# Optimization experiments

Measured on AMD Instinct MI355X. Metric: run time of the kernel, lower is better.

The kernel has to match this reference:

```python
import jax, jax.numpy as jnp
import numpy as np

D = 1024
H = 16
HD = D // H
S = 2048
B = 4
EPS = 1e-5


def gelu_tanh(x):
    c = jnp.sqrt(2.0 / jnp.pi).astype(x.dtype)
    return 0.5 * x * (1.0 + jnp.tanh(c * (x + 0.044715 * x ** 3)))


def layernorm(x, gamma, beta):
    mu = jnp.mean(x, axis=-1, keepdims=True)
    var = jnp.var(x, axis=-1, keepdims=True)
    return (x - mu) * jax.lax.rsqrt(var + EPS) * gamma + beta


def setup_inputs() -> dict:
    key = jax.random.key(0)
    ks = jax.random.split(key, 12)
    s = 0.02
    return {
        "x": jax.random.normal(ks[0], (B, S, D), jnp.float32),
        "Wq": jax.random.normal(ks[1], (D, D), jnp.float32) * s,
        "Wk": jax.random.normal(ks[2], (D, D), jnp.float32) * s,
        "Wv": jax.random.normal(ks[3], (D, D), jnp.float32) * s,
        "Wo": jax.random.normal(ks[4], (D, D), jnp.float32) * s,
        "bo": jnp.zeros((D,), jnp.float32),
        "W1": jax.random.normal(ks[5], (D, 4 * D), jnp.float32) * s,
        "b1": jnp.zeros((4 * D,), jnp.float32),
        "W2": jax.random.normal(ks[6], (4 * D, D), jnp.float32) * s,
        "b2": jnp.zeros((D,), jnp.float32),
        "g1": jnp.ones((D,), jnp.float32),
        "be1": jnp.zeros((D,), jnp.float32),
        "g2": jnp.ones((D,), jnp.float32),
        "be2": jnp.zeros((D,), jnp.float32),
    }


def reference(x, Wq, Wk, Wv, Wo, bo, W1, b1, W2, b2, g1, be1, g2, be2):
    b, n, d = x.shape
    # --- attention sub-block (pre-LN) ---
    h = layernorm(x, g1, be1)
    q = (h @ Wq).reshape(b, n, H, HD).transpose(0, 2, 1, 3)  # [b,H,n,hd]
    k = (h @ Wk).reshape(b, n, H, HD).transpose(0, 2, 1, 3)
    v = (h @ Wv).reshape(b, n, H, HD).transpose(0, 2, 1, 3)
    scores = jnp.einsum('bhqd,bhkd->bhqk', q, k) / jnp.sqrt(jnp.float32(HD))
    causal = jnp.tril(jnp.ones((n, n), dtype=bool))
    scores = jnp.where(causal, scores, -jnp.inf)
    w = jax.nn.softmax(scores, axis=-1)  # dropout rate 0 -> identity
    attn = jnp.einsum('bhqk,bhkd->bhqd', w, v)
    attn = attn.transpose(0, 2, 1, 3).reshape(b, n, d)
    x = x + (attn @ Wo + bo)
    # --- FFN sub-block (pre-LN) ---
    h = layernorm(x, g2, be2)
    h = gelu_tanh(h @ W1 + b1) @ W2 + b2
    return x + h
```

## Files before the change

kernel.cpp:

```cpp
#include <hip/hip_runtime.h>
#include <hip/hip_bf16.h>
#include <math.h>


typedef __attribute__((ext_vector_type(8))) short bf16x8;
typedef __attribute__((ext_vector_type(4))) float f32x4;

#define AS1 __attribute__((address_space(1)))
#define AS3 __attribute__((address_space(3)))

__device__ __forceinline__ void gl_lds16(const void* g, void* l) {
  __builtin_amdgcn_global_load_lds((const AS1 void*)g, (AS3 void*)l, 16, 0, 0);
}

__device__ __forceinline__ float gelu_f(float x) {
  const float c = 0.7978845608028654f;
  return 0.5f * x * (1.0f + tanhf(c * (x + 0.044715f * x * x * x)));
}

__device__ __forceinline__ float bf2f(short s) {
  unsigned u = ((unsigned)(unsigned short)s) << 16;
  return __builtin_bit_cast(float, u);
}
__device__ __forceinline__ short f2bf(float f) {
  __hip_bfloat16 h = __float2bfloat16(f);
  return __builtin_bit_cast(short, h);
}

__global__ void __launch_bounds__(256) tcvt_all(
    const float* __restrict__ Wq, const float* __restrict__ Wk,
    const float* __restrict__ Wv, const float* __restrict__ Wo,
    const float* __restrict__ W1, const float* __restrict__ W2,
    __hip_bfloat16* __restrict__ WqkvT, __hip_bfloat16* __restrict__ WoT,
    __hip_bfloat16* __restrict__ W1T, __hip_bfloat16* __restrict__ W2T) {
  __shared__ float t[32][33];
  const int bid = blockIdx.x;
  const float* W;
  __hip_bfloat16* WT;
  int K, N, n0, k0;
  if (bid < 4096) {
    const int which = bid >> 10, r = bid & 1023;
    K = 1024; N = 1024;
    n0 = (r & 31) * 32; k0 = (r >> 5) * 32;
    W = which == 0 ? Wq : which == 1 ? Wk : which == 2 ? Wv : Wo;
    WT = which < 3 ? WqkvT + which * 1024 * 1024 : WoT;
  } else if (bid < 8192) {
    const int r = bid - 4096;
    K = 1024; N = 4096;
    n0 = (r & 127) * 32; k0 = (r >> 7) * 32;
    W = W1; WT = W1T;
  } else {
    const int r = bid - 8192;
    K = 4096; N = 1024;
    n0 = (r & 31) * 32; k0 = (r >> 5) * 32;
    W = W2; WT = W2T;
  }
  const int tx = threadIdx.x, ty0 = threadIdx.y;
#pragma unroll
  for (int i = 0; i < 4; i++) {
    int ty = ty0 + i * 8;
    t[ty][tx] = W[(size_t)(k0 + ty) * N + n0 + tx];
  }
  __syncthreads();
#pragma unroll
  for (int i = 0; i < 4; i++) {
    int ty = ty0 + i * 8;
    WT[(size_t)(n0 + ty) * K + k0 + tx] = __float2bfloat16(t[tx][ty]);
  }
}

__global__ void __launch_bounds__(256) vtr_kernel(
    const __hip_bfloat16* __restrict__ qkv, __hip_bfloat16* __restrict__ vt) {
  __shared__ __hip_bfloat16 t[32][33];
  const int s0 = blockIdx.x * 32;
  const int hd0 = blockIdx.y * 32;
  const int bh = blockIdx.z;
  const int b = bh >> 4, h = bh & 15;
  const int tx = threadIdx.x, ty0 = threadIdx.y;
  const __hip_bfloat16* src =
      qkv + (size_t)(b * 2048 + s0) * 3072 + 2048 + h * 64 + hd0;
#pragma unroll
  for (int i = 0; i < 4; i++) {
    int ty = ty0 + i * 8;
    t[ty][tx] = src[(size_t)ty * 3072 + tx];
  }
  __syncthreads();
  __hip_bfloat16* dst = vt + ((size_t)bh * 64 + hd0) * 2048 + s0;
#pragma unroll
  for (int i = 0; i < 4; i++) {
    int ty = ty0 + i * 8;
    dst[(size_t)ty * 2048 + tx] = t[tx][ty];
  }
}

__global__ void __launch_bounds__(256) ln_kernel(
    const float* __restrict__ x, const float* __restrict__ gma,
    const float* __restrict__ bta, __hip_bfloat16* __restrict__ out) {
  const int row = blockIdx.x;
  const int tid = threadIdx.x;
  const float4 v = ((const float4*)(x + (size_t)row * 1024))[tid];
  float s = v.x + v.y + v.z + v.w;
  float s2 = v.x * v.x + v.y * v.y + v.z * v.z + v.w * v.w;
#pragma unroll
  for (int m = 32; m; m >>= 1) {
    s += __shfl_xor(s, m);
    s2 += __shfl_xor(s2, m);
  }
  __shared__ float red[8];
  const int w = tid >> 6, lane = tid & 63;
  if (lane == 0) { red[w] = s; red[4 + w] = s2; }
  __syncthreads();
  s = red[0] + red[1] + red[2] + red[3];
  s2 = red[4] + red[5] + red[6] + red[7];
  const float mu = s * (1.0f / 1024.0f);
  const float var = s2 * (1.0f / 1024.0f) - mu * mu;
  const float rs = rsqrtf(var + 1e-5f);
  const float4 gv = ((const float4*)gma)[tid];
  const float4 bv = ((const float4*)bta)[tid];
  __hip_bfloat16* orow = out + (size_t)row * 1024 + tid * 4;
  orow[0] = __float2bfloat16((v.x - mu) * rs * gv.x + bv.x);
  orow[1] = __float2bfloat16((v.y - mu) * rs * gv.y + bv.y);
  orow[2] = __float2bfloat16((v.z - mu) * rs * gv.z + bv.z);
  orow[3] = __float2bfloat16((v.w - mu) * rs * gv.w + bv.w);
}

template <int BM, int BN, int EPI>
__global__ void __launch_bounds__(512, 2) gemm8(
    const __hip_bfloat16* __restrict__ Ap, const __hip_bfloat16* __restrict__ Bp,
    void* __restrict__ outp, const float* __restrict__ bias,
    const float* __restrict__ resid, int N, int K) {
  constexpr int PM = BM / 2;
  constexpr int MR = PM / 16;
  constexpr int NPH = MR / 2;
  constexpr int HA = BM / 128;
  constexpr int ABYTES = BM * 128;
  constexpr int BUFB = ABYTES + BN * 128;
  __shared__ __attribute__((aligned(128))) char smem[2 * BUFB];

  const int tid = threadIdx.x;
  const int lane = tid & 63, w = tid >> 6;
  const int wr = w >> 2, wc = w & 3;
  const int cr = lane & 15, g = lane >> 4;

  const int gx = gridDim.x;
  const int nwg = gx * gridDim.y;
  const int orig = blockIdx.y * gx + blockIdx.x;
  const int f = (orig & 7) * (nwg >> 3) + (orig >> 3);
  const int sid = f >> 4, wit = f & 15;
  const int stm = gx >> 2;
  const int bm = (sid % stm) * 4 + (wit & 3);
  const int bn = (sid / stm) * 4 + (wit >> 2);
  const int bmr = bm * BM, bnr = bn * BN;
  const int nkt = K >> 6;

  const int srow8 = lane >> 3;
  const int ssl = ((lane & 7) ^ srow8) * 8;
  unsigned aofs[2][2], bofs[2][2];
#pragma unroll
  for (int h = 0; h < 2; h++)
#pragma unroll
    for (int c = 0; c < 2; c++) {
      const int ha = (h < HA) ? h : 0;
      aofs[h][c] =
          (unsigned)(((bmr + ha * 128 + (w + c * 8) * 8 + srow8) * K + ssl) * 2);
      bofs[h][c] =
          (unsigned)(((bnr + h * 128 + (w + c * 8) * 8 + srow8) * K + ssl) * 2);
    }

  const int rk = cr & 7;
  const char* aP[2][2];
  const char* bP[2][2];
#pragma unroll
  for (int bf = 0; bf < 2; bf++)
#pragma unroll
    for (int ks = 0; ks < 2; ks++) {
      aP[bf][ks] =
          smem + bf * BUFB + (wr * PM + cr) * 128 + ((ks * 4 + g) ^ rk) * 16;
      bP[bf][ks] = smem + bf * BUFB + ABYTES + (wc * 64 + cr) * 128 +
                   ((ks * 4 + g) ^ rk) * 16;
    }

#define STG_A(BUF, tt, h)                                                     \
  do {                                                                        \
    const unsigned col = (unsigned)(tt) * 128u;                               \
    gl_lds16((const char*)Ap + aofs[h][0] + col,                              \
             smem + (BUF) * BUFB + (h) * 16384 + w * 1024);                   \
    gl_lds16((const char*)Ap + aofs[h][1] + col,                              \
             smem + (BUF) * BUFB + (h) * 16384 + (w + 8) * 1024);             \
  } while (0)
#define STG_B(BUF, tt, h)                                                     \
  do {                                                                        \
    const unsigned col = (unsigned)(tt) * 128u;                               \
    gl_lds16((const char*)Bp + bofs[h][0] + col,                              \
             smem + (BUF) * BUFB + ABYTES + (h) * 16384 + w * 1024);          \
    gl_lds16((const char*)Bp + bofs[h][1] + col,                              \
             smem + (BUF) * BUFB + ABYTES + (h) * 16384 + (w + 8) * 1024);    \
  } while (0)

  f32x4 acc[MR][4];
#pragma unroll
  for (int i = 0; i < MR; i++)
#pragma unroll
    for (int j = 0; j < 4; j++) acc[i][j] = (f32x4){0.f, 0.f, 0.f, 0.f};
  bf16x8 bv[4][2];

#pragma unroll
  for (int h = 0; h < HA; h++) STG_A(0, 0, h);
  STG_B(0, 0, 0); STG_B(0, 0, 1);
  STG_B(1, 1, 0); STG_B(1, 1, 1);

#define TILE_BODY(BUF, t)                                                     \
  {                                                                           \
    asm volatile("s_waitcnt vmcnt(4)" ::: "memory");                          \
    __builtin_amdgcn_s_barrier();                                             \
    const int tA = ((t) + 1 < nkt) ? (t) + 1 : (t) - 1;                       \
    const int tB = ((t) + 2 < nkt) ? (t) + 2 : (t);                           \
    _Pragma("unroll") for (int q = 0; q < NPH; q++) {                         \
      bf16x8 av[2][2];                                                        \
      _Pragma("unroll") for (int mm = 0; mm < 2; mm++)                        \
          _Pragma("unroll") for (int ks = 0; ks < 2; ks++) av[mm][ks] =       \
          *(const bf16x8*)(aP[BUF][ks] + (q * 2 + mm) * 2048);                \
      if (q == 0) {                                                           \
        _Pragma("unroll") for (int n = 0; n < 4; n++)                         \
            _Pragma("unroll") for (int ks = 0; ks < 2; ks++) bv[n][ks] =      \
            *(const bf16x8*)(bP[BUF][ks] + n * 2048);                         \
      }                                                                       \
      if constexpr (NPH == 4) {                                               \
        if (q == 0) { STG_A((BUF) ^ 1, tA, 0); }                              \
        else if (q == 1) { STG_A((BUF) ^ 1, tA, 1); }                         \
        else if (q == 2) { STG_B(BUF, tB, 0); }                               \
        else { STG_B(BUF, tB, 1); }                                           \
      } else {                                                                \
        if (q == 0) { STG_A((BUF) ^ 1, tA, 0); }                              \
        else { STG_B(BUF, tB, 0); STG_B(BUF, tB, 1); }                        \
      }                                                                       \
      __builtin_amdgcn_s_barrier();                                           \
      asm volatile("s_waitcnt lgkmcnt(0)" ::: "memory");                      \
      __builtin_amdgcn_s_setprio(1);                                          \
      _Pragma("unroll") for (int mm = 0; mm < 2; mm++)                        \
          _Pragma("unroll") for (int n = 0; n < 4; n++)                       \
              _Pragma("unroll") for (int ks = 0; ks < 2; ks++)                \
                  acc[q * 2 + mm][n] =                                        \
          __builtin_amdgcn_mfma_f32_16x16x32_bf16(av[mm][ks], bv[n][ks],      \
                                                  acc[q * 2 + mm][n], 0, 0, 0); \
      __builtin_amdgcn_s_setprio(0);                                          \
    }                                                                         \
  }

  for (int t = 0; t < nkt; t += 2) {
    TILE_BODY(0, t)
    TILE_BODY(1, t + 1)
  }
  asm volatile("s_waitcnt vmcnt(0)" ::: "memory");

#pragma unroll
  for (int m = 0; m < MR; m++) {
#pragma unroll
    for (int rr = 0; rr < 4; rr++) {
      const int row = bmr + wr * PM + m * 16 + g * 4 + rr;
#pragma unroll
      for (int n = 0; n < 4; n++) {
        const int col = bnr + wc * 64 + n * 16 + cr;
        float v = acc[m][n][rr];
        if (EPI == 0) {
          ((__hip_bfloat16*)outp)[(size_t)row * N + col] = __float2bfloat16(v);
        } else if (EPI == 1) {
          v += bias[col] + resid[(size_t)row * N + col];
          ((float*)outp)[(size_t)row * N + col] = v;
        } else {
          v = gelu_f(v + bias[col]);
          ((__hip_bfloat16*)outp)[(size_t)row * N + col] = __float2bfloat16(v);
        }
      }
    }
  }
#undef STG_A
#undef STG_B
#undef TILE_BODY
}

template <int EPI>
__global__ void __launch_bounds__(256) gemm97(
    const __hip_bfloat16* __restrict__ Ap, const __hip_bfloat16* __restrict__ Bp,
    void* __restrict__ outp, const float* __restrict__ bias,
    const float* __restrict__ resid, int N, int K) {
  __shared__ __hip_bfloat16 sA[128 * 64];
  __shared__ __hip_bfloat16 sB[128 * 64];
  const int tid = threadIdx.x;
  const int lane = tid & 63, w = tid >> 6;
  const int wr = w >> 1, wc = w & 1;
  const int cr = lane & 15, g = lane >> 4;

  const int gx = gridDim.x;
  const int nwg = gx * gridDim.y;
  const int orig = blockIdx.y * gx + blockIdx.x;
  const int f = (orig & 7) * (nwg >> 3) + (orig >> 3);
  const int sid = f >> 4, wit = f & 15;
  const int stm = gx >> 2;
  const int bm = (sid % stm) * 4 + (wit & 3);
  const int bn = (sid / stm) * 4 + (wit >> 2);
  const int bmr = bm * 128, bnr = bn * 128;

  const int l8 = lane >> 3;
  const int ssl = ((lane & 7) ^ l8) * 8;
  const int rk = cr & 7;

  f32x4 acc[4][4];
#pragma unroll
  for (int i = 0; i < 4; i++)
#pragma unroll
    for (int j = 0; j < 4; j++) acc[i][j] = (f32x4){0.f, 0.f, 0.f, 0.f};

  for (int k0 = 0; k0 < K; k0 += 64) {
#pragma unroll
    for (int i = 0; i < 4; i++) {
      const int chunk = w * 4 + i;
      const int row = chunk * 8 + l8;
      gl_lds16(Ap + (size_t)(bmr + row) * K + k0 + ssl, sA + chunk * 512);
      gl_lds16(Bp + (size_t)(bnr + row) * K + k0 + ssl, sB + chunk * 512);
    }
    __syncthreads();
#pragma unroll
    for (int ks = 0; ks < 2; ks++) {
      bf16x8 a[4], b[4];
#pragma unroll
      for (int m = 0; m < 4; m++)
        a[m] = *(const bf16x8*)(sA + (wr * 64 + m * 16 + cr) * 64 +
                                ((ks * 4 + g) ^ rk) * 8);
#pragma unroll
      for (int n = 0; n < 4; n++)
        b[n] = *(const bf16x8*)(sB + (wc * 64 + n * 16 + cr) * 64 +
                                ((ks * 4 + g) ^ rk) * 8);
#pragma unroll
      for (int m = 0; m < 4; m++)
#pragma unroll
        for (int n = 0; n < 4; n++)
          acc[m][n] =
              __builtin_amdgcn_mfma_f32_16x16x32_bf16(a[m], b[n], acc[m][n], 0, 0, 0);
    }
    __syncthreads();
  }

#pragma unroll
  for (int m = 0; m < 4; m++) {
#pragma unroll
    for (int rr = 0; rr < 4; rr++) {
      const int row = bmr + wr * 64 + m * 16 + g * 4 + rr;
#pragma unroll
      for (int n = 0; n < 4; n++) {
        const int col = bnr + wc * 64 + n * 16 + cr;
        float v = acc[m][n][rr];
        if (EPI == 0) {
          ((__hip_bfloat16*)outp)[(size_t)row * N + col] = __float2bfloat16(v);
        } else if (EPI == 1) {
          v += bias[col] + resid[(size_t)row * N + col];
          ((float*)outp)[(size_t)row * N + col] = v;
        } else {
          v = gelu_f(v + bias[col]);
          ((__hip_bfloat16*)outp)[(size_t)row * N + col] = __float2bfloat16(v);
        }
      }
    }
  }
}

__global__ void __launch_bounds__(256) attn_kernel(
    const __hip_bfloat16* __restrict__ qkv, const __hip_bfloat16* __restrict__ vt,
    __hip_bfloat16* __restrict__ o) {
  __shared__ __hip_bfloat16 sK[2][64 * 64];
  __shared__ __hip_bfloat16 sV[2][64 * 64];
  __shared__ __hip_bfloat16 pl[4][16][64];
  const int tid = threadIdx.x, lane = tid & 63, w = tid >> 6;
  const int bid = blockIdx.x;
  const int bh = (bid & 7) + 8 * ((bid >> 3) & 7);
  const int qt = 15 - (bid >> 6);
  const int b = bh >> 4, h = bh & 15;
  const int cr = lane & 15, g = lane >> 4;
  const int qr0 = qt * 128 + w * 32;
  const float NEG = -1e30f;
  const float SC2 = 0.18033688011112042f;
  const int sw = cr & 7;
  const int sg0 = (g ^ sw) * 8;
  const int sg1 = ((g ^ sw) ^ 4) * 8;
  const int pkey = (cr & 7) << 1;

  bf16x8 aq[2][2];
#pragma unroll
  for (int m = 0; m < 2; m++) {
    const __hip_bfloat16* qp =
        qkv + (size_t)(b * 2048 + qr0 + m * 16 + cr) * 3072 + h * 64 + g * 8;
    bf16x8 q0 = *(const bf16x8*)qp;
    bf16x8 q1 = *(const bf16x8*)(qp + 32);
#pragma unroll
    for (int j = 0; j < 8; j++) {
      aq[m][0][j] = f2bf(bf2f(q0[j]) * SC2);
      aq[m][1][j] = f2bf(bf2f(q1[j]) * SC2);
    }
  }
  const __hip_bfloat16* kbase = qkv + (size_t)(b * 2048) * 3072 + 1024 + h * 64;
  const __hip_bfloat16* vbase = vt + (size_t)bh * 64 * 2048;

  const int l8 = lane >> 3, c8 = lane & 7;
  const int c8s = (c8 ^ l8) * 8;
#define STAGE_TILE(bi, ktile)                                                   \
  {                                                                             \
    _Pragma("unroll") for (int i = 0; i < 2; i++) {                             \
      const int rb = (i * 4 + w) * 8 + l8;                                      \
      gl_lds16(kbase + (size_t)((ktile) * 64 + rb) * 3072 + c8s,                \
               &sK[bi][(i * 4 + w) * 512]);                                     \
      gl_lds16(vbase + (size_t)rb * 2048 + (ktile) * 64 + c8s,                  \
               &sV[bi][(i * 4 + w) * 512]);                                     \
    }                                                                           \
  }

  f32x4 oacc[2][4];
#pragma unroll
  for (int m = 0; m < 2; m++)
#pragma unroll
    for (int i = 0; i < 4; i++) oacc[m][i] = (f32x4){0.f, 0.f, 0.f, 0.f};
  float mrow[2] = {NEG, NEG};
  float lrow[2] = {0.f, 0.f};

  const int nkt = (qt + 1) * 2;
  STAGE_TILE(0, 0);
  asm volatile("s_waitcnt vmcnt(0)" ::: "memory");
  __syncthreads();
  int cur = 0;

  for (int kt = 0; kt < nkt; ++kt) {
    if (kt + 1 < nkt) STAGE_TILE(cur ^ 1, kt + 1);

    if (kt * 64 <= qr0 + 31) {
      f32x4 st[4][2];
      __builtin_amdgcn_s_setprio(1);
#pragma unroll
      for (int kf = 0; kf < 4; kf++) {
        const bf16x8 bk0 = *(const bf16x8*)&sK[cur][(kf * 16 + cr) * 64 + sg0];
        const bf16x8 bk1 = *(const bf16x8*)&sK[cur][(kf * 16 + cr) * 64 + sg1];
#pragma unroll
        for (int mq = 0; mq < 2; mq++) {
          f32x4 z = (f32x4){0.f, 0.f, 0.f, 0.f};
          z = __builtin_amdgcn_mfma_f32_16x16x32_bf16(bk0, aq[mq][0], z, 0, 0, 0);
          z = __builtin_amdgcn_mfma_f32_16x16x32_bf16(bk1, aq[mq][1], z, 0, 0, 0);
          st[kf][mq] = z;
        }
      }
      __builtin_amdgcn_s_setprio(0);
      if (kt * 64 + 63 > qr0) {
#pragma unroll
        for (int kf = 0; kf < 4; kf++)
#pragma unroll
          for (int mq = 0; mq < 2; mq++)
#pragma unroll
            for (int rr = 0; rr < 4; rr++) {
              const int kvcol = kt * 64 + kf * 16 + g * 4 + rr;
              const int qrow = qr0 + mq * 16 + cr;
              if (kvcol > qrow) st[kf][mq][rr] = NEG;
            }
      }
#pragma unroll
      for (int mq = 0; mq < 2; mq++) {
        float pmax = st[0][mq][0];
#pragma unroll
        for (int kf = 0; kf < 4; kf++)
#pragma unroll
          for (int rr = 0; rr < 4; rr++)
            pmax = fmaxf(pmax, st[kf][mq][rr]);
        pmax = fmaxf(pmax, __shfl_xor(pmax, 16));
        pmax = fmaxf(pmax, __shfl_xor(pmax, 32));
        if (__any(pmax > mrow[mq] + 8.0f)) {
          const float mn = fmaxf(mrow[mq], pmax);
          const float scl = exp2f(mrow[mq] - mn);
          mrow[mq] = mn;
          lrow[mq] *= scl;
          float s0 = __shfl(scl, g * 4 + 0);
          float s1 = __shfl(scl, g * 4 + 1);
          float s2 = __shfl(scl, g * 4 + 2);
          float s3 = __shfl(scl, g * 4 + 3);
#pragma unroll
          for (int nf = 0; nf < 4; nf++) {
            f32x4 t = oacc[mq][nf];
            t[0] *= s0; t[1] *= s1; t[2] *= s2; t[3] *= s3;
            oacc[mq][nf] = t;
          }
        }
        float rsum = 0.f;
#pragma unroll
        for (int kf = 0; kf < 4; kf++) {
          short4 pk;
#pragma unroll
          for (int rr = 0; rr < 4; rr++) {
            const float p = exp2f(st[kf][mq][rr] - mrow[mq]);
            rsum += p;
            ((short*)&pk)[rr] = f2bf(p);
          }
          const int slot4 = (kf * 4 + g) ^ pkey;
          *(short4*)&pl[w][cr][slot4 * 4] = pk;
        }
        rsum += __shfl_xor(rsum, 16);
        rsum += __shfl_xor(rsum, 32);
        lrow[mq] += rsum;
        const bf16x8 pa0 = *(const bf16x8*)&pl[w][cr][((2 * g) ^ pkey) * 4];
        const bf16x8 pa1 = *(const bf16x8*)&pl[w][cr][((2 * g + 8) ^ pkey) * 4];
        __builtin_amdgcn_s_setprio(1);
#pragma unroll
        for (int nf = 0; nf < 4; nf++) {
          const bf16x8 bv0 = *(const bf16x8*)&sV[cur][(nf * 16 + cr) * 64 + sg0];
          const bf16x8 bv1 = *(const bf16x8*)&sV[cur][(nf * 16 + cr) * 64 + sg1];
          oacc[mq][nf] = __builtin_amdgcn_mfma_f32_16x16x32_bf16(pa0, bv0, oacc[mq][nf], 0, 0, 0);
          oacc[mq][nf] = __builtin_amdgcn_mfma_f32_16x16x32_bf16(pa1, bv1, oacc[mq][nf], 0, 0, 0);
        }
        __builtin_amdgcn_s_setprio(0);
      }
    }

    if (kt + 1 < nkt) {
      asm volatile("s_waitcnt vmcnt(0)" ::: "memory");
      __syncthreads();
      cur ^= 1;
    }
  }

#pragma unroll
  for (int m = 0; m < 2; m++) {
    float il[4];
#pragma unroll
    for (int rr = 0; rr < 4; rr++)
      il[rr] = 1.0f / __shfl(lrow[m], g * 4 + rr);
#pragma unroll
    for (int nf = 0; nf < 4; nf++)
#pragma unroll
      for (int rr = 0; rr < 4; rr++) {
        const int row = qr0 + m * 16 + g * 4 + rr;
        o[(size_t)(b * 2048 + row) * 1024 + h * 64 + nf * 16 + cr] =
            __float2bfloat16(oacc[m][nf][rr] * il[rr]);
      }
  }
#undef STAGE_TILE
}

extern "C" void kernel_launch(void* const* d_in, const int* in_sizes, int n_in,
                              void* d_out, int out_size, void* d_ws, size_t ws_size,
                              hipStream_t stream) {
  const float* x   = (const float*)d_in[0];
  const float* Wq  = (const float*)d_in[1];
  const float* Wk  = (const float*)d_in[2];
  const float* Wv  = (const float*)d_in[3];
  const float* Wo  = (const float*)d_in[4];
  const float* bo  = (const float*)d_in[5];
  const float* W1  = (const float*)d_in[6];
  const float* b1  = (const float*)d_in[7];
  const float* W2  = (const float*)d_in[8];
  const float* b2  = (const float*)d_in[9];
  const float* g1  = (const float*)d_in[10];
  const float* be1 = (const float*)d_in[11];
  const float* g2  = (const float*)d_in[12];
  const float* be2 = (const float*)d_in[13];

  char* ws = (char*)d_ws;
  const size_t MB = 1024 * 1024;
  __hip_bfloat16* hA    = (__hip_bfloat16*)(ws + 0);
  __hip_bfloat16* attnO = (__hip_bfloat16*)(ws + 0);
  __hip_bfloat16* qkv   = (__hip_bfloat16*)(ws + 16 * MB);
  float*          x2    = (float*)(ws + 16 * MB);
  __hip_bfloat16* h2    = (__hip_bfloat16*)(ws + 48 * MB);
  __hip_bfloat16* vtg   = (__hip_bfloat16*)(ws + 64 * MB);
  __hip_bfloat16* act   = (__hip_bfloat16*)(ws + 64 * MB);
  __hip_bfloat16* WqkvT = (__hip_bfloat16*)(ws + 128 * MB);
  __hip_bfloat16* WoT   = (__hip_bfloat16*)(ws + 134 * MB);
  __hip_bfloat16* W1T   = (__hip_bfloat16*)(ws + 136 * MB);
  __hip_bfloat16* W2T   = (__hip_bfloat16*)(ws + 144 * MB);

  const dim3 tb(32, 8);
  tcvt_all<<<12288, tb, 0, stream>>>(Wq, Wk, Wv, Wo, W1, W2,
                                     WqkvT, WoT, W1T, W2T);

  ln_kernel<<<8192, 256, 0, stream>>>(x, g1, be1, hA);
  gemm8<128, 256, 0><<<dim3(64, 12), 512, 0, stream>>>(
      hA, WqkvT, qkv, nullptr, nullptr, 3072, 1024);
  vtr_kernel<<<dim3(64, 2, 64), tb, 0, stream>>>(qkv, vtg);
  attn_kernel<<<1024, 256, 0, stream>>>(qkv, vtg, attnO);
  gemm8<128, 256, 1><<<dim3(64, 4), 512, 0, stream>>>(
      attnO, WoT, x2, bo, x, 1024, 1024);
  ln_kernel<<<8192, 256, 0, stream>>>(x2, g2, be2, h2);
  gemm8<256, 256, 2><<<dim3(32, 16), 512, 0, stream>>>(
      h2, W1T, act, b1, nullptr, 4096, 1024);
  gemm97<1><<<dim3(64, 8), 256, 0, stream>>>(
      act, W2T, (float*)d_out, b2, x2, 1024, 4096);
  (void)in_sizes; (void)n_in; (void)out_size; (void)ws_size;
}
```

Measured before the change: 389.1 us.

## Replace pipelined gemm8 with simple gemm97 and retile attention to 256-row blocks

```diff
diff --git a/kernel.cpp b/kernel.cpp
--- a/kernel.cpp
+++ b/kernel.cpp
@@ -124,22 +124,16 @@
   orow[3] = __float2bfloat16((v.w - mu) * rs * gv.w + bv.w);
 }
 
-template <int BM, int BN, int EPI>
-__global__ void __launch_bounds__(512, 2) gemm8(
+template <int EPI>
+__global__ void __launch_bounds__(256) gemm97(
     const __hip_bfloat16* __restrict__ Ap, const __hip_bfloat16* __restrict__ Bp,
     void* __restrict__ outp, const float* __restrict__ bias,
     const float* __restrict__ resid, int N, int K) {
-  constexpr int PM = BM / 2;
-  constexpr int MR = PM / 16;
-  constexpr int NPH = MR / 2;
-  constexpr int HA = BM / 128;
-  constexpr int ABYTES = BM * 128;
-  constexpr int BUFB = ABYTES + BN * 128;
-  __shared__ __attribute__((aligned(128))) char smem[2 * BUFB];
-
+  __shared__ __hip_bfloat16 sA[128 * 64];
+  __shared__ __hip_bfloat16 sB[128 * 64];
   const int tid = threadIdx.x;
   const int lane = tid & 63, w = tid >> 6;
-  const int wr = w >> 2, wc = w & 3;
+  const int wr = w >> 1, wc = w & 1;
   const int cr = lane & 15, g = lane >> 4;
 
   const int gx = gridDim.x;
@@ -150,114 +144,53 @@
   const int stm = gx >> 2;
   const int bm = (sid % stm) * 4 + (wit & 3);
   const int bn = (sid / stm) * 4 + (wit >> 2);
-  const int bmr = bm * BM, bnr = bn * BN;
-  const int nkt = K >> 6;
-
-  const int srow8 = lane >> 3;
-  const int ssl = ((lane & 7) ^ srow8) * 8;
-  unsigned aofs[2][2], bofs[2][2];
-#pragma unroll
-  for (int h = 0; h < 2; h++)
-#pragma unroll
-    for (int c = 0; c < 2; c++) {
-      const int ha = (h < HA) ? h : 0;
-      aofs[h][c] =
-          (unsigned)(((bmr + ha * 128 + (w + c * 8) * 8 + srow8) * K + ssl) * 2);
-      bofs[h][c] =
-          (unsigned)(((bnr + h * 128 + (w + c * 8) * 8 + srow8) * K + ssl) * 2);
-    }
-
+  const int bmr = bm * 128, bnr = bn * 128;
+
+  const int l8 = lane >> 3;
+  const int ssl = ((lane & 7) ^ l8) * 8;
   const int rk = cr & 7;
-  const char* aP[2][2];
-  const char* bP[2][2];
-#pragma unroll
-  for (int bf = 0; bf < 2; bf++)
+
+  f32x4 acc[4][4];
+#pragma unroll
+  for (int i = 0; i < 4; i++)
+#pragma unroll
+    for (int j = 0; j < 4; j++) acc[i][j] = (f32x4){0.f, 0.f, 0.f, 0.f};
+
+  for (int k0 = 0; k0 < K; k0 += 64) {
+#pragma unroll
+    for (int i = 0; i < 4; i++) {
+      const int chunk = w * 4 + i;
+      const int row = chunk * 8 + l8;
+      gl_lds16(Ap + (size_t)(bmr + row) * K + k0 + ssl, sA + chunk * 512);
+      gl_lds16(Bp + (size_t)(bnr + row) * K + k0 + ssl, sB + chunk * 512);
+    }
+    __syncthreads();
 #pragma unroll
     for (int ks = 0; ks < 2; ks++) {
-      aP[bf][ks] =
-          smem + bf * BUFB + (wr * PM + cr) * 128 + ((ks * 4 + g) ^ rk) * 16;
-      bP[bf][ks] = smem + bf * BUFB + ABYTES + (wc * 64 + cr) * 128 +
-                   ((ks * 4 + g) ^ rk) * 16;
-    }
-
-#define STG_A(BUF, tt, h)                                                     \
-  do {                                                                        \
-    const unsigned col = (unsigned)(tt) * 128u;                               \
-    gl_lds16((const char*)Ap + aofs[h][0] + col,                              \
-             smem + (BUF) * BUFB + (h) * 16384 + w * 1024);                   \
-    gl_lds16((const char*)Ap + aofs[h][1] + col,                              \
-             smem + (BUF) * BUFB + (h) * 16384 + (w + 8) * 1024);             \
-  } while (0)
-#define STG_B(BUF, tt, h)                                                     \
-  do {                                                                        \
-    const unsigned col = (unsigned)(tt) * 128u;                               \
-    gl_lds16((const char*)Bp + bofs[h][0] + col,                              \
-             smem + (BUF) * BUFB + ABYTES + (h) * 16384 + w * 1024);          \
-    gl_lds16((const char*)Bp + bofs[h][1] + col,                              \
-             smem + (BUF) * BUFB + ABYTES + (h) * 16384 + (w + 8) * 1024);    \
-  } while (0)
-
-  f32x4 acc[MR][4];
-#pragma unroll
-  for (int i = 0; i < MR; i++)
-#pragma unroll
-    for (int j = 0; j < 4; j++) acc[i][j] = (f32x4){0.f, 0.f, 0.f, 0.f};
-  bf16x8 bv[4][2];
-
-#pragma unroll
-  for (int h = 0; h < HA; h++) STG_A(0, 0, h);
-  STG_B(0, 0, 0); STG_B(0, 0, 1);
-  STG_B(1, 1, 0); STG_B(1, 1, 1);
-
-#define TILE_BODY(BUF, t)                                                     \
-  {                                                                           \
-    asm volatile("s_waitcnt vmcnt(4)" ::: "memory");                          \
-    __builtin_amdgcn_s_barrier();                                             \
-    const int tA = ((t) + 1 < nkt) ? (t) + 1 : (t) - 1;                       \
-    const int tB = ((t) + 2 < nkt) ? (t) + 2 : (t);                           \
-    _Pragma("unroll") for (int q = 0; q < NPH; q++) {                         \
-      bf16x8 av[2][2];                                                        \
-      _Pragma("unroll") for (int mm = 0; mm < 2; mm++)                        \
-          _Pragma("unroll") for (int ks = 0; ks < 2; ks++) av[mm][ks] =       \
-          *(const bf16x8*)(aP[BUF][ks] + (q * 2 + mm) * 2048);                \
-      if (q == 0) {                                                           \
-        _Pragma("unroll") for (int n = 0; n < 4; n++)                         \
-            _Pragma("unroll") for (int ks = 0; ks < 2; ks++) bv[n][ks] =      \
-            *(const bf16x8*)(bP[BUF][ks] + n * 2048);                         \
-      }                                                                       \
-      if constexpr (NPH == 4) {                                               \
-        if (q == 0) { STG_A((BUF) ^ 1, tA, 0); }                              \
-        else if (q == 1) { STG_A((BUF) ^ 1, tA, 1); }                         \
-        else if (q == 2) { STG_B(BUF, tB, 0); }                               \
-        else { STG_B(BUF, tB, 1); }                                           \
-      } else {                                                                \
-        if (q == 0) { STG_A((BUF) ^ 1, tA, 0); }                              \
-        else { STG_B(BUF, tB, 0); STG_B(BUF, tB, 1); }                        \
-      }                                                                       \
-      __builtin_amdgcn_s_barrier();                                           \
-      asm volatile("s_waitcnt lgkmcnt(0)" ::: "memory");                      \
-      __builtin_amdgcn_s_setprio(1);                                          \
-      _Pragma("unroll") for (int mm = 0; mm < 2; mm++)                        \
-          _Pragma("unroll") for (int n = 0; n < 4; n++)                       \
-              _Pragma("unroll") for (int ks = 0; ks < 2; ks++)                \
-                  acc[q * 2 + mm][n] =                                        \
-          __builtin_amdgcn_mfma_f32_16x16x32_bf16(av[mm][ks], bv[n][ks],      \
-                                                  acc[q * 2 + mm][n], 0, 0, 0); \
-      __builtin_amdgcn_s_setprio(0);                                          \
-    }                                                                         \
-  }
-
-  for (int t = 0; t < nkt; t += 2) {
-    TILE_BODY(0, t)
-    TILE_BODY(1, t + 1)
-  }
-  asm volatile("s_waitcnt vmcnt(0)" ::: "memory");
-
-#pragma unroll
-  for (int m = 0; m < MR; m++) {
+      bf16x8 a[4], b[4];
+#pragma unroll
+      for (int m = 0; m < 4; m++)
+        a[m] = *(const bf16x8*)(sA + (wr * 64 + m * 16 + cr) * 64 +
+                                ((ks * 4 + g) ^ rk) * 8);
+#pragma unroll
+      for (int n = 0; n < 4; n++)
+        b[n] = *(const bf16x8*)(sB + (wc * 64 + n * 16 + cr) * 64 +
+                                ((ks * 4 + g) ^ rk) * 8);
+#pragma unroll
+      for (int m = 0; m < 4; m++)
+#pragma unroll
+        for (int n = 0; n < 4; n++)
+          acc[m][n] =
+              __builtin_amdgcn_mfma_f32_16x16x32_bf16(a[m], b[n], acc[m][n], 0, 0, 0);
+    }
+    __syncthreads();
+  }
+
+#pragma unroll
+  for (int m = 0; m < 4; m++) {
 #pragma unroll
     for (int rr = 0; rr < 4; rr++) {
-      const int row = bmr + wr * PM + m * 16 + g * 4 + rr;
+      const int row = bmr + wr * 64 + m * 16 + g * 4 + rr;
 #pragma unroll
       for (int n = 0; n < 4; n++) {
         const int col = bnr + wc * 64 + n * 16 + cr;
@@ -274,109 +207,23 @@
       }
     }
   }
-#undef STG_A
-#undef STG_B
-#undef TILE_BODY
-}
-
-template <int EPI>
-__global__ void __launch_bounds__(256) gemm97(
-    const __hip_bfloat16* __restrict__ Ap, const __hip_bfloat16* __restrict__ Bp,
-    void* __restrict__ outp, const float* __restrict__ bias,
-    const float* __restrict__ resid, int N, int K) {
-  __shared__ __hip_bfloat16 sA[128 * 64];
-  __shared__ __hip_bfloat16 sB[128 * 64];
-  const int tid = threadIdx.x;
-  const int lane = tid & 63, w = tid >> 6;
-  const int wr = w >> 1, wc = w & 1;
-  const int cr = lane & 15, g = lane >> 4;
-
-  const int gx = gridDim.x;
-  const int nwg = gx * gridDim.y;
-  const int orig = blockIdx.y * gx + blockIdx.x;
-  const int f = (orig & 7) * (nwg >> 3) + (orig >> 3);
-  const int sid = f >> 4, wit = f & 15;
-  const int stm = gx >> 2;
-  const int bm = (sid % stm) * 4 + (wit & 3);
-  const int bn = (sid / stm) * 4 + (wit >> 2);
-  const int bmr = bm * 128, bnr = bn * 128;
-
-  const int l8 = lane >> 3;
-  const int ssl = ((lane & 7) ^ l8) * 8;
-  const int rk = cr & 7;
-
-  f32x4 acc[4][4];
-#pragma unroll
-  for (int i = 0; i < 4; i++)
-#pragma unroll
-    for (int j = 0; j < 4; j++) acc[i][j] = (f32x4){0.f, 0.f, 0.f, 0.f};
-
-  for (int k0 = 0; k0 < K; k0 += 64) {
-#pragma unroll
-    for (int i = 0; i < 4; i++) {
-      const int chunk = w * 4 + i;
-      const int row = chunk * 8 + l8;
-      gl_lds16(Ap + (size_t)(bmr + row) * K + k0 + ssl, sA + chunk * 512);
-      gl_lds16(Bp + (size_t)(bnr + row) * K + k0 + ssl, sB + chunk * 512);
-    }
-    __syncthreads();
-#pragma unroll
-    for (int ks = 0; ks < 2; ks++) {
-      bf16x8 a[4], b[4];
-#pragma unroll
-      for (int m = 0; m < 4; m++)
-        a[m] = *(const bf16x8*)(sA + (wr * 64 + m * 16 + cr) * 64 +
-                                ((ks * 4 + g) ^ rk) * 8);
-#pragma unroll
-      for (int n = 0; n < 4; n++)
-        b[n] = *(const bf16x8*)(sB + (wc * 64 + n * 16 + cr) * 64 +
-                                ((ks * 4 + g) ^ rk) * 8);
-#pragma unroll
-      for (int m = 0; m < 4; m++)
-#pragma unroll
-        for (int n = 0; n < 4; n++)
-          acc[m][n] =
-              __builtin_amdgcn_mfma_f32_16x16x32_bf16(a[m], b[n], acc[m][n], 0, 0, 0);
-    }
-    __syncthreads();
-  }
-
-#pragma unroll
-  for (int m = 0; m < 4; m++) {
-#pragma unroll
-    for (int rr = 0; rr < 4; rr++) {
-      const int row = bmr + wr * 64 + m * 16 + g * 4 + rr;
-#pragma unroll
-      for (int n = 0; n < 4; n++) {
-        const int col = bnr + wc * 64 + n * 16 + cr;
-        float v = acc[m][n][rr];
-        if (EPI == 0) {
-          ((__hip_bfloat16*)outp)[(size_t)row * N + col] = __float2bfloat16(v);
-        } else if (EPI == 1) {
-          v += bias[col] + resid[(size_t)row * N + col];
-          ((float*)outp)[(size_t)row * N + col] = v;
-        } else {
-          v = gelu_f(v + bias[col]);
-          ((__hip_bfloat16*)outp)[(size_t)row * N + col] = __float2bfloat16(v);
-        }
-      }
-    }
-  }
-}
-
-__global__ void __launch_bounds__(256) attn_kernel(
+}
+
+__global__ void __launch_bounds__(512) attn_kernel(
     const __hip_bfloat16* __restrict__ qkv, const __hip_bfloat16* __restrict__ vt,
     __hip_bfloat16* __restrict__ o) {
   __shared__ __hip_bfloat16 sK[2][64 * 64];
   __shared__ __hip_bfloat16 sV[2][64 * 64];
-  __shared__ __hip_bfloat16 pl[4][16][64];
+  __shared__ __hip_bfloat16 pl[8][16][64];
   const int tid = threadIdx.x, lane = tid & 63, w = tid >> 6;
-  const int bid = blockIdx.x;
-  const int bh = (bid & 7) + 8 * ((bid >> 3) & 7);
-  const int qt = 15 - (bid >> 6);
+  const int orig = blockIdx.x;
+  const int f = (orig & 7) * 64 + (orig >> 3);
+  const int bh = f >> 3;
+  const int idx = f & 7;
+  const int qt = (idx & 1) ? (idx >> 1) : (7 - (idx >> 1));
   const int b = bh >> 4, h = bh & 15;
   const int cr = lane & 15, g = lane >> 4;
-  const int qr0 = qt * 128 + w * 32;
+  const int qr0 = qt * 256 + w * 32;
   const float NEG = -1e30f;
   const float SC2 = 0.18033688011112042f;
   const int sw = cr & 7;
@@ -402,15 +249,13 @@
 
   const int l8 = lane >> 3, c8 = lane & 7;
   const int c8s = (c8 ^ l8) * 8;
+  const int rb = w * 8 + l8;
 #define STAGE_TILE(bi, ktile)                                                   \
   {                                                                             \
-    _Pragma("unroll") for (int i = 0; i < 2; i++) {                             \
-      const int rb = (i * 4 + w) * 8 + l8;                                      \
-      gl_lds16(kbase + (size_t)((ktile) * 64 + rb) * 3072 + c8s,                \
-               &sK[bi][(i * 4 + w) * 512]);                                     \
-      gl_lds16(vbase + (size_t)rb * 2048 + (ktile) * 64 + c8s,                  \
-               &sV[bi][(i * 4 + w) * 512]);                                     \
-    }                                                                           \
+    gl_lds16(kbase + (size_t)((ktile) * 64 + rb) * 3072 + c8s,                  \
+             &sK[bi][w * 512]);                                                 \
+    gl_lds16(vbase + (size_t)rb * 2048 + (ktile) * 64 + c8s,                    \
+             &sV[bi][w * 512]);                                                 \
   }
 
   f32x4 oacc[2][4];
@@ -421,7 +266,7 @@
   float mrow[2] = {NEG, NEG};
   float lrow[2] = {0.f, 0.f};
 
-  const int nkt = (qt + 1) * 2;
+  const int nkt = (qt + 1) * 4;
   STAGE_TILE(0, 0);
   asm volatile("s_waitcnt vmcnt(0)" ::: "memory");
   __syncthreads();
@@ -457,6 +302,12 @@
               const int qrow = qr0 + mq * 16 + cr;
               if (kvcol > qrow) st[kf][mq][rr] = NEG;
             }
+      }
+      bf16x8 bvv0[4], bvv1[4];
+#pragma unroll
+      for (int nf = 0; nf < 4; nf++) {
+        bvv0[nf] = *(const bf16x8*)&sV[cur][(nf * 16 + cr) * 64 + sg0];
+        bvv1[nf] = *(const bf16x8*)&sV[cur][(nf * 16 + cr) * 64 + sg1];
       }
 #pragma unroll
       for (int mq = 0; mq < 2; mq++) {
@@ -505,10 +356,8 @@
         __builtin_amdgcn_s_setprio(1);
 #pragma unroll
         for (int nf = 0; nf < 4; nf++) {
-          const bf16x8 bv0 = *(const bf16x8*)&sV[cur][(nf * 16 + cr) * 64 + sg0];
-          const bf16x8 bv1 = *(const bf16x8*)&sV[cur][(nf * 16 + cr) * 64 + sg1];
-          oacc[mq][nf] = __builtin_amdgcn_mfma_f32_16x16x32_bf16(pa0, bv0, oacc[mq][nf], 0, 0, 0);
-          oacc[mq][nf] = __builtin_amdgcn_mfma_f32_16x16x32_bf16(pa1, bv1, oacc[mq][nf], 0, 0, 0);
+          oacc[mq][nf] = __builtin_amdgcn_mfma_f32_16x16x32_bf16(pa0, bvv0[nf], oacc[mq][nf], 0, 0, 0);
+          oacc[mq][nf] = __builtin_amdgcn_mfma_f32_16x16x32_bf16(pa1, bvv1[nf], oacc[mq][nf], 0, 0, 0);
         }
         __builtin_amdgcn_s_setprio(0);
       }
@@ -576,14 +425,14 @@
                                      WqkvT, WoT, W1T, W2T);
 
   ln_kernel<<<8192, 256, 0, stream>>>(x, g1, be1, hA);
-  gemm8<128, 256, 0><<<dim3(64, 12), 512, 0, stream>>>(
+  gemm97<0><<<dim3(64, 24), 256, 0, stream>>>(
       hA, WqkvT, qkv, nullptr, nullptr, 3072, 1024);
   vtr_kernel<<<dim3(64, 2, 64), tb, 0, stream>>>(qkv, vtg);
-  attn_kernel<<<1024, 256, 0, stream>>>(qkv, vtg, attnO);
-  gemm8<128, 256, 1><<<dim3(64, 4), 512, 0, stream>>>(
+  attn_kernel<<<512, 512, 0, stream>>>(qkv, vtg, attnO);
+  gemm97<1><<<dim3(64, 8), 256, 0, stream>>>(
       attnO, WoT, x2, bo, x, 1024, 1024);
   ln_kernel<<<8192, 256, 0, stream>>>(x2, g2, be2, h2);
-  gemm8<256, 256, 2><<<dim3(32, 16), 512, 0, stream>>>(
+  gemm97<2><<<dim3(64, 32), 256, 0, stream>>>(
       h2, W1T, act, b1, nullptr, 4096, 1024);
   gemm97<1><<<dim3(64, 8), 256, 0, stream>>>(
       act, W2T, (float*)d_out, b2, x2, 1024, 4096);
```

Measured after the change: 458.6 us. +17.9%, slower.
